# Optimization experiments

Hardware: AMD Instinct MI355X
Metric: run time of the kernel (lower is better)

The kernel has to match this reference:

```python
import jax, jax.numpy as jnp
import numpy as np

E = 1024  # hidden_size
H = 16    # num_heads
D = E // H  # head_dim = 64


def setup_inputs() -> dict:
    key = jax.random.key(0)
    ks = jax.random.split(key, 10)
    s = 1.0 / np.sqrt(E)
    inp = {
        "hidden_states": jax.random.normal(ks[0], (2, 2048, E), dtype=jnp.float32),
        "attention_mask": jnp.ones((2, 2048), dtype=jnp.float32),
        "Wq": jax.random.normal(ks[1], (E, E), dtype=jnp.float32) * s,
        "bq": jnp.zeros((E,), dtype=jnp.float32),
        "Wk": jax.random.normal(ks[2], (E, E), dtype=jnp.float32) * s,
        "bk": jnp.zeros((E,), dtype=jnp.float32),
        "Wv": jax.random.normal(ks[3], (E, E), dtype=jnp.float32) * s,
        "bv": jnp.zeros((E,), dtype=jnp.float32),
        "Wo": jax.random.normal(ks[4], (E, E), dtype=jnp.float32) * s,
        "bo": jnp.zeros((E,), dtype=jnp.float32),
    }
    return inp


def _split_heads(x):
    # [B, S, E] -> [B, H, S, D]
    b, s, _ = x.shape
    return x.reshape(b, s, H, D).transpose(0, 2, 1, 3)


def reference(hidden_states, attention_mask, Wq, bq, Wk, bk, Wv, bv, Wo, bo):
    b, s, _ = hidden_states.shape
    q = _split_heads(hidden_states @ Wq + bq)  # [B,H,S,D]
    k = _split_heads(hidden_states @ Wk + bk)
    v = _split_heads(hidden_states @ Wv + bv)
    scores = jnp.einsum('bhqd,bhkd->bhqk', q, k) / jnp.sqrt(jnp.float32(D))
    scores = scores + (1.0 - attention_mask)[:, None, None, :] * -10000.0
    probs = jax.nn.softmax(scores, axis=-1)
    ctx = jnp.einsum('bhqk,bhkd->bhqd', probs, v)  # [B,H,S,D]
    ctx = ctx.transpose(0, 2, 1, 3).reshape(b, s, E)
    return ctx @ Wo + bo
```

## Files before the change

kernel.cpp:

```cpp
#include <hip/hip_runtime.h>
#include <hip/hip_bf16.h>
#include <stdint.h>

typedef __bf16 bf16x8 __attribute__((ext_vector_type(8)));
typedef __bf16 bf16x4_t __attribute__((ext_vector_type(4)));
typedef float  f32x4  __attribute__((ext_vector_type(4)));
typedef short  short8 __attribute__((ext_vector_type(8)));
typedef short  short4v __attribute__((ext_vector_type(4)));
typedef float  float4v __attribute__((ext_vector_type(4)));

#define AS1 __attribute__((address_space(1)))
#define AS3 __attribute__((address_space(3)))

__device__ __forceinline__ void g2l16(const void* g, void* l) {
    __builtin_amdgcn_global_load_lds((const AS1 void*)g, (AS3 void*)l, 16, 0, 0);
}

__device__ __forceinline__ short f2bf(float f) {
    unsigned u = __builtin_bit_cast(unsigned, f);
    unsigned r = u + 0x7FFFu + ((u >> 16) & 1u);
    return (short)(r >> 16);
}

__device__ __forceinline__ bf16x8 ldb8(const short* p) {
    return __builtin_bit_cast(bf16x8, *(const short8*)p);
}

__device__ __forceinline__ float fast_exp2(float x) {
    return __builtin_amdgcn_exp2f(x);
}

#define LOG2E 1.44269504f
#define QSCL (0.125f * LOG2E)

__global__ __launch_bounds__(256) void prep(
    const float* __restrict__ X, short* __restrict__ Xb,
    const float* __restrict__ W0, const float* __restrict__ W1,
    const float* __restrict__ W2, const float* __restrict__ W3,
    short* __restrict__ T0, short* __restrict__ T1,
    short* __restrict__ T2, short* __restrict__ T3) {
    int gb = blockIdx.x;
    if (gb < 4096) {
        int i = (gb * 256 + threadIdx.x) * 4;
        float4v v = *(const float4v*)(X + i);
        short4v o;
        o[0] = f2bf(v[0]); o[1] = f2bf(v[1]); o[2] = f2bf(v[2]); o[3] = f2bf(v[3]);
        *(short4v*)(Xb + i) = o;
        return;
    }
    int t = gb - 4096;
    int z = t >> 10, rem = t & 1023;
    int xb = rem & 31, yb = rem >> 5;
    const float* W = z == 0 ? W0 : z == 1 ? W1 : z == 2 ? W2 : W3;
    short* T = z == 0 ? T0 : z == 1 ? T1 : z == 2 ? T2 : T3;
    __shared__ float tt[32][33];
    int n0 = xb * 32, k0 = yb * 32;
    int tx = threadIdx.x & 31, ty = threadIdx.x >> 5;
#pragma unroll
    for (int i = 0; i < 4; i++)
        tt[ty + i * 8][tx] = W[(size_t)(k0 + ty + i * 8) * 1024 + n0 + tx];
    __syncthreads();
#pragma unroll
    for (int i = 0; i < 4; i++)
        T[(size_t)(n0 + ty + i * 8) * 1024 + k0 + tx] = f2bf(tt[tx][ty + i * 8]);
}

#define VROW 136
__global__ __launch_bounds__(256) void gemm_qkv(
    const short* __restrict__ Xb,
    const short* __restrict__ WqT, const short* __restrict__ WkT, const short* __restrict__ WvT,
    const float* __restrict__ bq, const float* __restrict__ bk, const float* __restrict__ bv,
    short* __restrict__ Qb, short* __restrict__ Kb, short* __restrict__ VT) {
    const int K = 1024, N = 1024;
    int mt = blockIdx.x;
    int yy = blockIdx.y;
    int mat = yy >> 3, nt = yy & 7;
    const short* Bt = mat == 0 ? WqT : mat == 1 ? WkT : WvT;
    const float* bias = mat == 0 ? bq : mat == 1 ? bk : bv;

    int tid = threadIdx.x;
    int w = tid >> 6, lane = tid & 63;
    int quad = lane >> 4, l16 = lane & 15;
    int wy = w >> 1, wx = w & 1;

    __shared__ __align__(16) short smem[128 * VROW];
    short* A_lds = smem;
    short* B_lds = smem + 4096;

    f32x4 acc[4][4];
#pragma unroll
    for (int i = 0; i < 4; i++)
#pragma unroll
        for (int j = 0; j < 4; j++) acc[i][j] = (f32x4){0.f, 0.f, 0.f, 0.f};

    int m0 = mt * 128, n0 = nt * 128;

    if (mat < 2) {
        for (int kt = 0; kt < 32; kt++) {
            __syncthreads();
#pragma unroll
            for (int c = 0; c < 2; c++) {
                int row = w * 32 + c * 16 + (lane >> 2);
                g2l16(Xb + (size_t)(m0 + row) * K + kt * 32 + (lane & 3) * 8,
                      &A_lds[(w * 32 + c * 16) * 32]);
                g2l16(Bt + (size_t)(n0 + row) * K + kt * 32 + (lane & 3) * 8,
                      &B_lds[(w * 32 + c * 16) * 32]);
            }
            __syncthreads();
            bf16x8 af[4], bfr[4];
#pragma unroll
            for (int i = 0; i < 4; i++) {
                af[i]  = ldb8(&A_lds[(wy * 64 + i * 16 + l16) * 32 + quad * 8]);
                bfr[i] = ldb8(&B_lds[(wx * 64 + i * 16 + l16) * 32 + quad * 8]);
            }
#pragma unroll
            for (int ni = 0; ni < 4; ni++)
#pragma unroll
                for (int mi = 0; mi < 4; mi++)
                    acc[ni][mi] = __builtin_amdgcn_mfma_f32_16x16x32_bf16(bfr[ni], af[mi], acc[ni][mi], 0, 0, 0);
        }
        short* Cout = mat == 0 ? Qb : Kb;
        float s = mat == 0 ? QSCL : 1.0f;
#pragma unroll
        for (int ni = 0; ni < 4; ni++) {
            int c0 = n0 + wx * 64 + ni * 16 + quad * 4;
            float4v bv4 = *(const float4v*)(bias + c0);
#pragma unroll
            for (int mi = 0; mi < 4; mi++) {
                int row = m0 + wy * 64 + mi * 16 + l16;
                f32x4 a = acc[ni][mi];
                f32x4 av = {(a[0] + bv4[0]) * s, (a[1] + bv4[1]) * s,
                            (a[2] + bv4[2]) * s, (a[3] + bv4[3]) * s};
                bf16x4_t ob = __builtin_convertvector(av, bf16x4_t);
                *(short4v*)&Cout[(size_t)row * N + c0] = __builtin_bit_cast(short4v, ob);
            }
        }
    } else {
        for (int kt = 0; kt < 32; kt++) {
            __syncthreads();
#pragma unroll
            for (int c = 0; c < 2; c++) {
                int row = w * 32 + c * 16 + (lane >> 2);
                g2l16(Xb + (size_t)(m0 + row) * K + kt * 32 + (lane & 3) * 8,
                      &A_lds[(w * 32 + c * 16) * 32]);
                g2l16(Bt + (size_t)(n0 + row) * K + kt * 32 + (lane & 3) * 8,
                      &B_lds[(w * 32 + c * 16) * 32]);
            }
            __syncthreads();
            bf16x8 af[4], bfr[4];
#pragma unroll
            for (int i = 0; i < 4; i++) {
                af[i]  = ldb8(&A_lds[(wy * 64 + i * 16 + l16) * 32 + quad * 8]);
                bfr[i] = ldb8(&B_lds[(wx * 64 + i * 16 + l16) * 32 + quad * 8]);
            }
#pragma unroll
            for (int mi = 0; mi < 4; mi++)
#pragma unroll
                for (int ni = 0; ni < 4; ni++)
                    acc[mi][ni] = __builtin_amdgcn_mfma_f32_16x16x32_bf16(af[mi], bfr[ni], acc[mi][ni], 0, 0, 0);
        }
        __syncthreads();
#pragma unroll
        for (int ni = 0; ni < 4; ni++) {
            int cl = wx * 64 + ni * 16 + l16;
            float bv_ = bias[n0 + cl];
#pragma unroll
            for (int mi = 0; mi < 4; mi++) {
                int ml = wy * 64 + mi * 16 + quad * 4;
                f32x4 a = acc[mi][ni];
                f32x4 av = {a[0] + bv_, a[1] + bv_, a[2] + bv_, a[3] + bv_};
                bf16x4_t ob = __builtin_convertvector(av, bf16x4_t);
                *(short4v*)&smem[cl * VROW + ml] = __builtin_bit_cast(short4v, ob);
            }
        }
        __syncthreads();
        int bb = m0 >> 11, ss0 = m0 & 2047;
        int t16 = tid & 15, cw = tid >> 4;
#pragma unroll
        for (int p = 0; p < 8; p++) {
            int cl = p * 16 + cw;
            int col = n0 + cl;
            *(short8*)&VT[(((size_t)(bb * 16)) << 17) + (size_t)col * 2048 + ss0 + t16 * 8] =
                *(const short8*)&smem[cl * VROW + t16 * 8];
        }
    }
}

__global__ __launch_bounds__(256) void gemm_out(
    const short* __restrict__ Ab, const short* __restrict__ Bt,
    const float* __restrict__ bias, float* __restrict__ C) {
    const int K = 1024, N = 1024;
    int mt = blockIdx.x, nt = blockIdx.y;
    int tid = threadIdx.x;
    int w = tid >> 6, lane = tid & 63;
    int quad = lane >> 4, l16 = lane & 15;

    __shared__ __align__(16) short A_lds[64 * 32];
    __shared__ __align__(16) short B_lds[128 * 32];

    f32x4 acc[2][4];
#pragma unroll
    for (int ni = 0; ni < 2; ni++)
#pragma unroll
        for (int mi = 0; mi < 4; mi++) acc[ni][mi] = (f32x4){0.f, 0.f, 0.f, 0.f};

    int m0 = mt * 64, n0 = nt * 128;
    for (int kt = 0; kt < 32; kt++) {
        __syncthreads();
        {
            int row = w * 16 + (lane >> 2);
            g2l16(Ab + (size_t)(m0 + row) * K + kt * 32 + (lane & 3) * 8,
                  &A_lds[(w * 16) * 32]);
        }
#pragma unroll
        for (int c = 0; c < 2; c++) {
            int row = w * 32 + c * 16 + (lane >> 2);
            g2l16(Bt + (size_t)(n0 + row) * K + kt * 32 + (lane & 3) * 8,
                  &B_lds[(w * 32 + c * 16) * 32]);
        }
        __syncthreads();
        bf16x8 af[4], bfr[2];
#pragma unroll
        for (int i = 0; i < 4; i++)
            af[i] = ldb8(&A_lds[(i * 16 + l16) * 32 + quad * 8]);
#pragma unroll
        for (int i = 0; i < 2; i++)
            bfr[i] = ldb8(&B_lds[(w * 32 + i * 16 + l16) * 32 + quad * 8]);
#pragma unroll
        for (int ni = 0; ni < 2; ni++)
#pragma unroll
            for (int mi = 0; mi < 4; mi++)
                acc[ni][mi] = __builtin_amdgcn_mfma_f32_16x16x32_bf16(bfr[ni], af[mi], acc[ni][mi], 0, 0, 0);
    }
#pragma unroll
    for (int ni = 0; ni < 2; ni++) {
        int c0 = n0 + w * 32 + ni * 16 + quad * 4;
        float4v bv4 = *(const float4v*)(bias + c0);
#pragma unroll
        for (int mi = 0; mi < 4; mi++) {
            int row = m0 + mi * 16 + l16;
            f32x4 a = acc[ni][mi];
            float4v av = {a[0] + bv4[0], a[1] + bv4[1], a[2] + bv4[2], a[3] + bv4[3]};
            *(float4v*)&C[(size_t)row * N + c0] = av;
        }
    }
}

#define PROW 72
__global__ __launch_bounds__(512) void attn_kernel(
    const short* __restrict__ Qb, const short* __restrict__ Kb,
    const short* __restrict__ VT, const float* __restrict__ mask,
    short* __restrict__ ctx) {
    const int S = 2048, E = 1024, HH = 16;
    int g = blockIdx.x;
    int p = (g & 7) + 8 * (g >> 7);
    int qb = (g >> 3) & 15;
    int b = p >> 4, h = p & 15;

    int tid = threadIdx.x;
    int w = tid >> 6, lane = tid & 63;
    int quad = lane >> 4, l16 = lane & 15;

    __shared__ __align__(16) short K_lds[2][64 * 64];
    __shared__ __align__(16) short VT_lds[2][64 * 64];
    __shared__ __align__(16) short P_lds[8][16 * PROW];
    __shared__ int maskflag;

    if (tid == 0) maskflag = 1;
    __syncthreads();
    {
        float4v m = *(const float4v*)(mask + b * S + tid * 4);
        if (!(m[0] == 1.f && m[1] == 1.f && m[2] == 1.f && m[3] == 1.f))
            maskflag = 0;
    }
    __syncthreads();
    const bool nomask = (maskflag != 0);

    int q0 = qb * 128;

    bf16x8 qf[2];
#pragma unroll
    for (int kc = 0; kc < 2; kc++)
        qf[kc] = ldb8(Qb + (size_t)(b * S + q0 + w * 16 + l16) * E + h * 64 + kc * 32 + quad * 8);

    short8 ones_s = {0x3F80, 0x3F80, 0x3F80, 0x3F80, 0x3F80, 0x3F80, 0x3F80, 0x3F80};
    bf16x8 vones = __builtin_bit_cast(bf16x8, ones_s);

    f32x4 O_t[4];
    f32x4 lacc = (f32x4){0.f, 0.f, 0.f, 0.f};
#pragma unroll
    for (int nd = 0; nd < 4; nd++) O_t[nd] = (f32x4){0.f, 0.f, 0.f, 0.f};

    const short* Kbase = Kb + (size_t)b * S * E + h * 64;
    const short* Vbase = VT + (size_t)(b * HH + h) * 64 * S;
    short* Pw = &P_lds[w][0];
    int rsw = l16 & 7;

    int srow = w * 8 + (lane >> 3);
    int ssrcb = (lane & 7) ^ (srow & 7);

    g2l16(Kbase + (size_t)srow * E + ssrcb * 8, &K_lds[0][(w * 8) * 64]);
    g2l16(Vbase + (size_t)srow * S + 0 + ssrcb * 8, &VT_lds[0][(w * 8) * 64]);
    __syncthreads();

    for (int kt = 0; kt < 32; kt++) {
        int cur = kt & 1;
        int k0 = kt * 64;
        if (kt < 31) {
            int k1 = k0 + 64;
            g2l16(Kbase + (size_t)(k1 + srow) * E + ssrcb * 8, &K_lds[cur ^ 1][(w * 8) * 64]);
            g2l16(Vbase + (size_t)srow * S + k1 + ssrcb * 8, &VT_lds[cur ^ 1][(w * 8) * 64]);
        }
        const short* Kl = &K_lds[cur][0];
        const short* Vl = &VT_lds[cur][0];

        f32x4 sc[4];
#pragma unroll
        for (int ni = 0; ni < 4; ni++) sc[ni] = (f32x4){0.f, 0.f, 0.f, 0.f};
#pragma unroll
        for (int ni = 0; ni < 4; ni++) {
#pragma unroll
            for (int kc = 0; kc < 2; kc++) {
                int blk = (kc * 4 + quad) ^ rsw;
                bf16x8 kf = ldb8(&Kl[(ni * 16 + l16) * 64 + blk * 8]);
                sc[ni] = __builtin_amdgcn_mfma_f32_16x16x32_bf16(kf, qf[kc], sc[ni], 0, 0, 0);
            }
        }

        if (!nomask) {
#pragma unroll
            for (int ni = 0; ni < 4; ni++) {
                float4v mrow = *(const float4v*)(mask + b * S + k0 + ni * 16 + quad * 4);
#pragma unroll
                for (int r = 0; r < 4; r++)
                    sc[ni][r] += (1.0f - mrow[r]) * (-10000.0f * LOG2E);
            }
        }

#pragma unroll
        for (int ni = 0; ni < 4; ni++)
#pragma unroll
            for (int r = 0; r < 4; r++)
                sc[ni][r] = fast_exp2(sc[ni][r]);

#pragma unroll
        for (int ni = 0; ni < 4; ni++) {
            bf16x4_t pb = __builtin_convertvector(sc[ni], bf16x4_t);
            *(short4v*)&Pw[l16 * PROW + ni * 16 + quad * 4] =
                __builtin_bit_cast(short4v, pb);
        }

#pragma unroll
        for (int ks = 0; ks < 2; ks++) {
            bf16x8 pf = ldb8(&Pw[l16 * PROW + ks * 32 + quad * 8]);
            lacc = __builtin_amdgcn_mfma_f32_16x16x32_bf16(vones, pf, lacc, 0, 0, 0);
#pragma unroll
            for (int nd = 0; nd < 4; nd++) {
                int blk = (ks * 4 + quad) ^ rsw;
                bf16x8 vf = ldb8(&Vl[(nd * 16 + l16) * 64 + blk * 8]);
                O_t[nd] = __builtin_amdgcn_mfma_f32_16x16x32_bf16(vf, pf, O_t[nd], 0, 0, 0);
            }
        }
        __syncthreads();
    }

    {
        float l = lacc[0];
        float inv = l > 0.f ? 1.0f / l : 0.f;
        int row = q0 + w * 16 + l16;
#pragma unroll
        for (int nd = 0; nd < 4; nd++) {
            f32x4 o = O_t[nd];
            f32x4 os = {o[0] * inv, o[1] * inv, o[2] * inv, o[3] * inv};
            bf16x4_t ob = __builtin_convertvector(os, bf16x4_t);
            *(short4v*)&ctx[(size_t)(b * S + row) * E + h * 64 + nd * 16 + quad * 4] =
                __builtin_bit_cast(short4v, ob);
        }
    }
}

extern "C" void kernel_launch(void* const* d_in, const int* in_sizes, int n_in,
                              void* d_out, int out_size, void* d_ws, size_t ws_size,
                              hipStream_t stream) {
    const float* X    = (const float*)d_in[0];
    const float* mask = (const float*)d_in[1];
    const float* Wq   = (const float*)d_in[2];
    const float* bq   = (const float*)d_in[3];
    const float* Wk   = (const float*)d_in[4];
    const float* bk   = (const float*)d_in[5];
    const float* Wv   = (const float*)d_in[6];
    const float* bv   = (const float*)d_in[7];
    const float* Wo   = (const float*)d_in[8];
    const float* bo   = (const float*)d_in[9];
    float* out = (float*)d_out;

    char* ws = (char*)d_ws;
    short* Xb  = (short*)(ws);
    short* WqT = (short*)(ws + (8u << 20));
    short* WkT = (short*)(ws + (10u << 20));
    short* WvT = (short*)(ws + (12u << 20));
    short* WoT = (short*)(ws + (14u << 20));
    short* Qb  = (short*)(ws + (16u << 20));
    short* Kb  = (short*)(ws + (24u << 20));
    short* VT  = (short*)(ws + (32u << 20));
    short* ctx = Xb;

    prep<<<8192, 256, 0, stream>>>(X, Xb, Wq, Wk, Wv, Wo, WqT, WkT, WvT, WoT);
    gemm_qkv<<<dim3(32, 24), 256, 0, stream>>>(Xb, WqT, WkT, WvT, bq, bk, bv, Qb, Kb, VT);
    attn_kernel<<<512, 512, 0, stream>>>(Qb, Kb, VT, mask, ctx);
    gemm_out<<<dim3(64, 8), 256, 0, stream>>>(ctx, WoT, bo, out);
}
```

Measured before the change: 194.0 us.

## Switch attention to 32x32 MFMA tiles with split-K waves and LDS reduction

The attention kernel now uses 32x32x16 bf16 MFMAs instead of 16x16x32. Each wave covers 32 query rows and half of each 64-key tile: four query segments times two key halves across eight waves. The two key-half partial outputs and row sums are combined through an LDS reduction at the end, and the shared memory is unified into one buffer with a new P row pitch. This aims for better MFMA efficiency and fewer fragment loads per FLOP, at the cost of an extra reduction, more accumulator registers, and possible LDS bank conflicts from the new layout.

```diff
diff --git a/kernel.cpp b/kernel.cpp
--- a/kernel.cpp
+++ b/kernel.cpp
@@ -5,6 +5,7 @@
 typedef __bf16 bf16x8 __attribute__((ext_vector_type(8)));
 typedef __bf16 bf16x4_t __attribute__((ext_vector_type(4)));
 typedef float  f32x4  __attribute__((ext_vector_type(4)));
+typedef float  f32x16 __attribute__((ext_vector_type(16)));
 typedef short  short8 __attribute__((ext_vector_type(8)));
 typedef short  short4v __attribute__((ext_vector_type(4)));
 typedef float  float4v __attribute__((ext_vector_type(4)));
@@ -246,7 +247,7 @@
     }
 }
 
-#define PROW 72
+#define PR2 56
 __global__ __launch_bounds__(512) void attn_kernel(
     const short* __restrict__ Qb, const short* __restrict__ Kb,
     const short* __restrict__ VT, const float* __restrict__ mask,
@@ -259,11 +260,13 @@
 
     int tid = threadIdx.x;
     int w = tid >> 6, lane = tid & 63;
-    int quad = lane >> 4, l16 = lane & 15;
-
-    __shared__ __align__(16) short K_lds[2][64 * 64];
-    __shared__ __align__(16) short VT_lds[2][64 * 64];
-    __shared__ __align__(16) short P_lds[8][16 * PROW];
+    int l32 = lane & 31, hi = lane >> 5;
+    int qseg = w & 3, khalf = w >> 2;
+
+    __shared__ __align__(16) short smem_s[8192 + 8192 + 8 * 32 * PR2];
+    short* K_lds = smem_s;
+    short* V_lds = smem_s + 8192;
+    short* Pw = smem_s + 16384 + w * 32 * PR2;
     __shared__ int maskflag;
 
     if (tid == 0) maskflag = 1;
@@ -278,29 +281,28 @@
 
     int q0 = qb * 128;
 
-    bf16x8 qf[2];
-#pragma unroll
-    for (int kc = 0; kc < 2; kc++)
-        qf[kc] = ldb8(Qb + (size_t)(b * S + q0 + w * 16 + l16) * E + h * 64 + kc * 32 + quad * 8);
+    bf16x8 qf[4];
+#pragma unroll
+    for (int step = 0; step < 4; step++)
+        qf[step] = ldb8(Qb + (size_t)(b * S + q0 + qseg * 32 + l32) * E + h * 64 + step * 16 + hi * 8);
 
     short8 ones_s = {0x3F80, 0x3F80, 0x3F80, 0x3F80, 0x3F80, 0x3F80, 0x3F80, 0x3F80};
     bf16x8 vones = __builtin_bit_cast(bf16x8, ones_s);
 
-    f32x4 O_t[4];
-    f32x4 lacc = (f32x4){0.f, 0.f, 0.f, 0.f};
-#pragma unroll
-    for (int nd = 0; nd < 4; nd++) O_t[nd] = (f32x4){0.f, 0.f, 0.f, 0.f};
+    f32x16 O_t[2];
+    f32x16 lacc;
+#pragma unroll
+    for (int i = 0; i < 16; i++) { O_t[0][i] = 0.f; O_t[1][i] = 0.f; lacc[i] = 0.f; }
 
     const short* Kbase = Kb + (size_t)b * S * E + h * 64;
     const short* Vbase = VT + (size_t)(b * HH + h) * 64 * S;
-    short* Pw = &P_lds[w][0];
-    int rsw = l16 & 7;
 
     int srow = w * 8 + (lane >> 3);
     int ssrcb = (lane & 7) ^ (srow & 7);
-
-    g2l16(Kbase + (size_t)srow * E + ssrcb * 8, &K_lds[0][(w * 8) * 64]);
-    g2l16(Vbase + (size_t)srow * S + 0 + ssrcb * 8, &VT_lds[0][(w * 8) * 64]);
+    int l7 = lane & 7;
+
+    g2l16(Kbase + (size_t)srow * E + ssrcb * 8, &K_lds[(w * 8) * 64]);
+    g2l16(Vbase + (size_t)srow * S + 0 + ssrcb * 8, &V_lds[(w * 8) * 64]);
     __syncthreads();
 
     for (int kt = 0; kt < 32; kt++) {
@@ -308,73 +310,84 @@
         int k0 = kt * 64;
         if (kt < 31) {
             int k1 = k0 + 64;
-            g2l16(Kbase + (size_t)(k1 + srow) * E + ssrcb * 8, &K_lds[cur ^ 1][(w * 8) * 64]);
-            g2l16(Vbase + (size_t)srow * S + k1 + ssrcb * 8, &VT_lds[cur ^ 1][(w * 8) * 64]);
-        }
-        const short* Kl = &K_lds[cur][0];
-        const short* Vl = &VT_lds[cur][0];
-
-        f32x4 sc[4];
-#pragma unroll
-        for (int ni = 0; ni < 4; ni++) sc[ni] = (f32x4){0.f, 0.f, 0.f, 0.f};
-#pragma unroll
-        for (int ni = 0; ni < 4; ni++) {
-#pragma unroll
-            for (int kc = 0; kc < 2; kc++) {
-                int blk = (kc * 4 + quad) ^ rsw;
-                bf16x8 kf = ldb8(&Kl[(ni * 16 + l16) * 64 + blk * 8]);
-                sc[ni] = __builtin_amdgcn_mfma_f32_16x16x32_bf16(kf, qf[kc], sc[ni], 0, 0, 0);
-            }
+            g2l16(Kbase + (size_t)(k1 + srow) * E + ssrcb * 8, &K_lds[(cur ^ 1) * 4096 + (w * 8) * 64]);
+            g2l16(Vbase + (size_t)srow * S + k1 + ssrcb * 8, &V_lds[(cur ^ 1) * 4096 + (w * 8) * 64]);
+        }
+        const short* Kl = &K_lds[cur * 4096];
+        const short* Vl = &V_lds[cur * 4096];
+
+        f32x16 sc;
+#pragma unroll
+        for (int i = 0; i < 16; i++) sc[i] = 0.f;
+#pragma unroll
+        for (int step = 0; step < 4; step++) {
+            int blk = (step * 2 + hi) ^ l7;
+            bf16x8 kf = ldb8(&Kl[(khalf * 32 + l32) * 64 + blk * 8]);
+            sc = __builtin_amdgcn_mfma_f32_32x32x16_bf16(kf, qf[step], sc, 0, 0, 0);
         }
 
         if (!nomask) {
 #pragma unroll
-            for (int ni = 0; ni < 4; ni++) {
-                float4v mrow = *(const float4v*)(mask + b * S + k0 + ni * 16 + quad * 4);
+            for (int gg = 0; gg < 4; gg++) {
+                float4v mrow = *(const float4v*)(mask + b * S + k0 + khalf * 32 + gg * 8 + hi * 4);
 #pragma unroll
                 for (int r = 0; r < 4; r++)
-                    sc[ni][r] += (1.0f - mrow[r]) * (-10000.0f * LOG2E);
-            }
-        }
-
-#pragma unroll
-        for (int ni = 0; ni < 4; ni++)
-#pragma unroll
-            for (int r = 0; r < 4; r++)
-                sc[ni][r] = fast_exp2(sc[ni][r]);
-
-#pragma unroll
-        for (int ni = 0; ni < 4; ni++) {
-            bf16x4_t pb = __builtin_convertvector(sc[ni], bf16x4_t);
-            *(short4v*)&Pw[l16 * PROW + ni * 16 + quad * 4] =
-                __builtin_bit_cast(short4v, pb);
-        }
-
-#pragma unroll
-        for (int ks = 0; ks < 2; ks++) {
-            bf16x8 pf = ldb8(&Pw[l16 * PROW + ks * 32 + quad * 8]);
-            lacc = __builtin_amdgcn_mfma_f32_16x16x32_bf16(vones, pf, lacc, 0, 0, 0);
-#pragma unroll
-            for (int nd = 0; nd < 4; nd++) {
-                int blk = (ks * 4 + quad) ^ rsw;
-                bf16x8 vf = ldb8(&Vl[(nd * 16 + l16) * 64 + blk * 8]);
-                O_t[nd] = __builtin_amdgcn_mfma_f32_16x16x32_bf16(vf, pf, O_t[nd], 0, 0, 0);
+                    sc[gg * 4 + r] += (1.0f - mrow[r]) * (-10000.0f * LOG2E);
+            }
+        }
+
+#pragma unroll
+        for (int i = 0; i < 16; i++) sc[i] = fast_exp2(sc[i]);
+
+#pragma unroll
+        for (int gg = 0; gg < 4; gg++) {
+            f32x4 v4 = {sc[gg * 4 + 0], sc[gg * 4 + 1], sc[gg * 4 + 2], sc[gg * 4 + 3]};
+            bf16x4_t pb = __builtin_convertvector(v4, bf16x4_t);
+            *(short4v*)&Pw[l32 * PR2 + gg * 8 + hi * 4] = __builtin_bit_cast(short4v, pb);
+        }
+
+#pragma unroll
+        for (int step = 0; step < 2; step++) {
+            bf16x8 pf = ldb8(&Pw[l32 * PR2 + step * 16 + hi * 8]);
+            lacc = __builtin_amdgcn_mfma_f32_32x32x16_bf16(vones, pf, lacc, 0, 0, 0);
+#pragma unroll
+            for (int dseg = 0; dseg < 2; dseg++) {
+                int vblk = (khalf * 4 + step * 2 + hi) ^ l7;
+                bf16x8 vf = ldb8(&Vl[(dseg * 32 + l32) * 64 + vblk * 8]);
+                O_t[dseg] = __builtin_amdgcn_mfma_f32_32x32x16_bf16(vf, pf, O_t[dseg], 0, 0, 0);
             }
         }
         __syncthreads();
     }
 
-    {
-        float l = lacc[0];
+    float* Red = (float*)smem_s;
+    __syncthreads();
+    if (khalf == 1) {
+        float* r = &Red[(qseg * 64 + lane) * 33];
+#pragma unroll
+        for (int dseg = 0; dseg < 2; dseg++)
+#pragma unroll
+            for (int i = 0; i < 16; i++) r[dseg * 16 + i] = O_t[dseg][i];
+        r[32] = lacc[0];
+    }
+    __syncthreads();
+    if (khalf == 0) {
+        const float* r = &Red[(qseg * 64 + lane) * 33];
+        float l = lacc[0] + r[32];
         float inv = l > 0.f ? 1.0f / l : 0.f;
-        int row = q0 + w * 16 + l16;
-#pragma unroll
-        for (int nd = 0; nd < 4; nd++) {
-            f32x4 o = O_t[nd];
-            f32x4 os = {o[0] * inv, o[1] * inv, o[2] * inv, o[3] * inv};
-            bf16x4_t ob = __builtin_convertvector(os, bf16x4_t);
-            *(short4v*)&ctx[(size_t)(b * S + row) * E + h * 64 + nd * 16 + quad * 4] =
-                __builtin_bit_cast(short4v, ob);
+        int row = q0 + qseg * 32 + l32;
+#pragma unroll
+        for (int dseg = 0; dseg < 2; dseg++) {
+#pragma unroll
+            for (int gg = 0; gg < 4; gg++) {
+                f32x4 v4 = {(O_t[dseg][gg * 4 + 0] + r[dseg * 16 + gg * 4 + 0]) * inv,
+                            (O_t[dseg][gg * 4 + 1] + r[dseg * 16 + gg * 4 + 1]) * inv,
+                            (O_t[dseg][gg * 4 + 2] + r[dseg * 16 + gg * 4 + 2]) * inv,
+                            (O_t[dseg][gg * 4 + 3] + r[dseg * 16 + gg * 4 + 3]) * inv};
+                bf16x4_t ob = __builtin_convertvector(v4, bf16x4_t);
+                *(short4v*)&ctx[(size_t)(b * S + row) * E + h * 64 + dseg * 32 + gg * 8 + hi * 4] =
+                    __builtin_bit_cast(short4v, ob);
+            }
         }
     }
 }
```

After: 196.1 us. About the same (+1.1%).

## Double-buffer LDS tiles in projection GEMMs and pad attention P buffer

Applied to the files above, without the earlier changes.

Both the QKV and output GEMMs now use two LDS buffers, so the global-to-LDS load for tile k+1 is issued before the MFMAs on tile k. This replaces two barriers per iteration with one and is meant to hide load latency behind compute. The attention P scratch row stride changes from 72 to 76 shorts, with the 8-element fragment read as two 4-element loads, to reduce LDS bank conflicts. The trade-off is twice the LDS footprint per block, which may lower occupancy. The loop also relies on global_load_lds completing by the single barrier without an explicit vmcnt wait, which could be a correctness risk.

```diff
diff --git a/kernel.cpp b/kernel.cpp
--- a/kernel.cpp
+++ b/kernel.cpp
@@ -84,8 +84,6 @@
     int wy = w >> 1, wx = w & 1;
 
     __shared__ __align__(16) short smem[128 * VROW];
-    short* A_lds = smem;
-    short* B_lds = smem + 4096;
 
     f32x4 acc[4][4];
 #pragma unroll
@@ -94,30 +92,40 @@
         for (int j = 0; j < 4; j++) acc[i][j] = (f32x4){0.f, 0.f, 0.f, 0.f};
 
     int m0 = mt * 128, n0 = nt * 128;
+
+    auto stage = [&](int kt, short* A, short* B) {
+#pragma unroll
+        for (int c = 0; c < 2; c++) {
+            int row = w * 32 + c * 16 + (lane >> 2);
+            g2l16(Xb + (size_t)(m0 + row) * K + kt * 32 + (lane & 3) * 8,
+                  &A[(w * 32 + c * 16) * 32]);
+            g2l16(Bt + (size_t)(n0 + row) * K + kt * 32 + (lane & 3) * 8,
+                  &B[(w * 32 + c * 16) * 32]);
+        }
+    };
+
+    stage(0, smem, smem + 8192);
+    __syncthreads();
 
     if (mat < 2) {
         for (int kt = 0; kt < 32; kt++) {
-            __syncthreads();
-#pragma unroll
-            for (int c = 0; c < 2; c++) {
-                int row = w * 32 + c * 16 + (lane >> 2);
-                g2l16(Xb + (size_t)(m0 + row) * K + kt * 32 + (lane & 3) * 8,
-                      &A_lds[(w * 32 + c * 16) * 32]);
-                g2l16(Bt + (size_t)(n0 + row) * K + kt * 32 + (lane & 3) * 8,
-                      &B_lds[(w * 32 + c * 16) * 32]);
-            }
-            __syncthreads();
+            int cur = kt & 1;
+            const short* Al = cur ? smem + 4096 : smem;
+            const short* Bl = cur ? smem + 12288 : smem + 8192;
+            if (kt < 31)
+                stage(kt + 1, cur ? smem : smem + 4096, cur ? smem + 8192 : smem + 12288);
             bf16x8 af[4], bfr[4];
 #pragma unroll
             for (int i = 0; i < 4; i++) {
-                af[i]  = ldb8(&A_lds[(wy * 64 + i * 16 + l16) * 32 + quad * 8]);
-                bfr[i] = ldb8(&B_lds[(wx * 64 + i * 16 + l16) * 32 + quad * 8]);
+                af[i]  = ldb8(&Al[(wy * 64 + i * 16 + l16) * 32 + quad * 8]);
+                bfr[i] = ldb8(&Bl[(wx * 64 + i * 16 + l16) * 32 + quad * 8]);
             }
 #pragma unroll
             for (int ni = 0; ni < 4; ni++)
 #pragma unroll
                 for (int mi = 0; mi < 4; mi++)
                     acc[ni][mi] = __builtin_amdgcn_mfma_f32_16x16x32_bf16(bfr[ni], af[mi], acc[ni][mi], 0, 0, 0);
+            __syncthreads();
         }
         short* Cout = mat == 0 ? Qb : Kb;
         float s = mat == 0 ? QSCL : 1.0f;
@@ -137,29 +145,24 @@
         }
     } else {
         for (int kt = 0; kt < 32; kt++) {
-            __syncthreads();
-#pragma unroll
-            for (int c = 0; c < 2; c++) {
-                int row = w * 32 + c * 16 + (lane >> 2);
-                g2l16(Xb + (size_t)(m0 + row) * K + kt * 32 + (lane & 3) * 8,
-                      &A_lds[(w * 32 + c * 16) * 32]);
-                g2l16(Bt + (size_t)(n0 + row) * K + kt * 32 + (lane & 3) * 8,
-                      &B_lds[(w * 32 + c * 16) * 32]);
-            }
-            __syncthreads();
+            int cur = kt & 1;
+            const short* Al = cur ? smem + 4096 : smem;
+            const short* Bl = cur ? smem + 12288 : smem + 8192;
+            if (kt < 31)
+                stage(kt + 1, cur ? smem : smem + 4096, cur ? smem + 8192 : smem + 12288);
             bf16x8 af[4], bfr[4];
 #pragma unroll
             for (int i = 0; i < 4; i++) {
-                af[i]  = ldb8(&A_lds[(wy * 64 + i * 16 + l16) * 32 + quad * 8]);
-                bfr[i] = ldb8(&B_lds[(wx * 64 + i * 16 + l16) * 32 + quad * 8]);
+                af[i]  = ldb8(&Al[(wy * 64 + i * 16 + l16) * 32 + quad * 8]);
+                bfr[i] = ldb8(&Bl[(wx * 64 + i * 16 + l16) * 32 + quad * 8]);
             }
 #pragma unroll
             for (int mi = 0; mi < 4; mi++)
 #pragma unroll
                 for (int ni = 0; ni < 4; ni++)
                     acc[mi][ni] = __builtin_amdgcn_mfma_f32_16x16x32_bf16(af[mi], bfr[ni], acc[mi][ni], 0, 0, 0);
-        }
-        __syncthreads();
+            __syncthreads();
+        }
 #pragma unroll
         for (int ni = 0; ni < 4; ni++) {
             int cl = wx * 64 + ni * 16 + l16;
@@ -195,8 +198,7 @@
     int w = tid >> 6, lane = tid & 63;
     int quad = lane >> 4, l16 = lane & 15;
 
-    __shared__ __align__(16) short A_lds[64 * 32];
-    __shared__ __align__(16) short B_lds[128 * 32];
+    __shared__ __align__(16) short smem[12288];
 
     f32x4 acc[2][4];
 #pragma unroll
@@ -205,32 +207,43 @@
         for (int mi = 0; mi < 4; mi++) acc[ni][mi] = (f32x4){0.f, 0.f, 0.f, 0.f};
 
     int m0 = mt * 64, n0 = nt * 128;
-    for (int kt = 0; kt < 32; kt++) {
-        __syncthreads();
+
+    auto stage = [&](int kt, short* A, short* B) {
         {
             int row = w * 16 + (lane >> 2);
             g2l16(Ab + (size_t)(m0 + row) * K + kt * 32 + (lane & 3) * 8,
-                  &A_lds[(w * 16) * 32]);
+                  &A[(w * 16) * 32]);
         }
 #pragma unroll
         for (int c = 0; c < 2; c++) {
             int row = w * 32 + c * 16 + (lane >> 2);
             g2l16(Bt + (size_t)(n0 + row) * K + kt * 32 + (lane & 3) * 8,
-                  &B_lds[(w * 32 + c * 16) * 32]);
-        }
-        __syncthreads();
+                  &B[(w * 32 + c * 16) * 32]);
+        }
+    };
+
+    stage(0, smem, smem + 4096);
+    __syncthreads();
+
+    for (int kt = 0; kt < 32; kt++) {
+        int cur = kt & 1;
+        const short* Al = cur ? smem + 2048 : smem;
+        const short* Bl = cur ? smem + 8192 : smem + 4096;
+        if (kt < 31)
+            stage(kt + 1, cur ? smem : smem + 2048, cur ? smem + 4096 : smem + 8192);
         bf16x8 af[4], bfr[2];
 #pragma unroll
         for (int i = 0; i < 4; i++)
-            af[i] = ldb8(&A_lds[(i * 16 + l16) * 32 + quad * 8]);
+            af[i] = ldb8(&Al[(i * 16 + l16) * 32 + quad * 8]);
 #pragma unroll
         for (int i = 0; i < 2; i++)
-            bfr[i] = ldb8(&B_lds[(w * 32 + i * 16 + l16) * 32 + quad * 8]);
+            bfr[i] = ldb8(&Bl[(w * 32 + i * 16 + l16) * 32 + quad * 8]);
 #pragma unroll
         for (int ni = 0; ni < 2; ni++)
 #pragma unroll
             for (int mi = 0; mi < 4; mi++)
                 acc[ni][mi] = __builtin_amdgcn_mfma_f32_16x16x32_bf16(bfr[ni], af[mi], acc[ni][mi], 0, 0, 0);
+        __syncthreads();
     }
 #pragma unroll
     for (int ni = 0; ni < 2; ni++) {
@@ -246,7 +259,7 @@
     }
 }
 
-#define PROW 72
+#define PROW 76
 __global__ __launch_bounds__(512) void attn_kernel(
     const short* __restrict__ Qb, const short* __restrict__ Kb,
     const short* __restrict__ VT, const float* __restrict__ mask,
@@ -352,7 +365,10 @@
 
 #pragma unroll
         for (int ks = 0; ks < 2; ks++) {
-            bf16x8 pf = ldb8(&Pw[l16 * PROW + ks * 32 + quad * 8]);
+            short4v p0 = *(const short4v*)&Pw[l16 * PROW + ks * 32 + quad * 8];
+            short4v p1 = *(const short4v*)&Pw[l16 * PROW + ks * 32 + quad * 8 + 4];
+            short8 pc = {p0[0], p0[1], p0[2], p0[3], p1[0], p1[1], p1[2], p1[3]};
+            bf16x8 pf = __builtin_bit_cast(bf16x8, pc);
             lacc = __builtin_amdgcn_mfma_f32_16x16x32_bf16(vones, pf, lacc, 0, 0, 0);
 #pragma unroll
             for (int nd = 0; nd < 4; nd++) {
```

Measured after the change: 195.4 us. No clear change (+0.7%).

## Double GEMM K-tile to 64 with XOR-swizzled LDS and pad attention P rows

Applied to the files above, without the earlier changes.

Both projection GEMMs now stage 64-wide K tiles into LDS, using an XOR swizzle on 16-byte blocks, so they run half as many barrier-separated iterations. The swizzle is meant to avoid LDS bank conflicts on the fragment reads. The duplicated Q/K and V main loops are merged into one loop that branches on the matrix type. In attention, the P row stride goes from 72 to 76 and P fragments are read as two 8-byte loads, aiming to cut bank conflicts at the cost of losing 16-byte aligned reads.

```diff
diff --git a/kernel.cpp b/kernel.cpp
--- a/kernel.cpp
+++ b/kernel.cpp
@@ -82,10 +82,11 @@
     int w = tid >> 6, lane = tid & 63;
     int quad = lane >> 4, l16 = lane & 15;
     int wy = w >> 1, wx = w & 1;
+    int rsw = l16 & 7;
 
     __shared__ __align__(16) short smem[128 * VROW];
     short* A_lds = smem;
-    short* B_lds = smem + 4096;
+    short* B_lds = smem + 8192;
 
     f32x4 acc[4][4];
 #pragma unroll
@@ -94,31 +95,46 @@
         for (int j = 0; j < 4; j++) acc[i][j] = (f32x4){0.f, 0.f, 0.f, 0.f};
 
     int m0 = mt * 128, n0 = nt * 128;
+    int srow8 = lane >> 3;
+    int ssrcb = (lane & 7) ^ srow8;
+
+    for (int kt = 0; kt < 16; kt++) {
+        __syncthreads();
+#pragma unroll
+        for (int c = 0; c < 4; c++) {
+            int row = w * 32 + c * 8 + srow8;
+            g2l16(Xb + (size_t)(m0 + row) * K + kt * 64 + ssrcb * 8,
+                  &A_lds[(w * 32 + c * 8) * 64]);
+            g2l16(Bt + (size_t)(n0 + row) * K + kt * 64 + ssrcb * 8,
+                  &B_lds[(w * 32 + c * 8) * 64]);
+        }
+        __syncthreads();
+#pragma unroll
+        for (int kc = 0; kc < 2; kc++) {
+            int blk = (kc * 4 + quad) ^ rsw;
+            bf16x8 af[4], bfr[4];
+#pragma unroll
+            for (int i = 0; i < 4; i++) {
+                af[i]  = ldb8(&A_lds[(wy * 64 + i * 16 + l16) * 64 + blk * 8]);
+                bfr[i] = ldb8(&B_lds[(wx * 64 + i * 16 + l16) * 64 + blk * 8]);
+            }
+            if (mat < 2) {
+#pragma unroll
+                for (int ni = 0; ni < 4; ni++)
+#pragma unroll
+                    for (int mi = 0; mi < 4; mi++)
+                        acc[ni][mi] = __builtin_amdgcn_mfma_f32_16x16x32_bf16(bfr[ni], af[mi], acc[ni][mi], 0, 0, 0);
+            } else {
+#pragma unroll
+                for (int mi = 0; mi < 4; mi++)
+#pragma unroll
+                    for (int ni = 0; ni < 4; ni++)
+                        acc[mi][ni] = __builtin_amdgcn_mfma_f32_16x16x32_bf16(af[mi], bfr[ni], acc[mi][ni], 0, 0, 0);
+            }
+        }
+    }
 
     if (mat < 2) {
-        for (int kt = 0; kt < 32; kt++) {
-            __syncthreads();
-#pragma unroll
-            for (int c = 0; c < 2; c++) {
-                int row = w * 32 + c * 16 + (lane >> 2);
-                g2l16(Xb + (size_t)(m0 + row) * K + kt * 32 + (lane & 3) * 8,
-                      &A_lds[(w * 32 + c * 16) * 32]);
-                g2l16(Bt + (size_t)(n0 + row) * K + kt * 32 + (lane & 3) * 8,
-                      &B_lds[(w * 32 + c * 16) * 32]);
-            }
-            __syncthreads();
-            bf16x8 af[4], bfr[4];
-#pragma unroll
-            for (int i = 0; i < 4; i++) {
-                af[i]  = ldb8(&A_lds[(wy * 64 + i * 16 + l16) * 32 + quad * 8]);
-                bfr[i] = ldb8(&B_lds[(wx * 64 + i * 16 + l16) * 32 + quad * 8]);
-            }
-#pragma unroll
-            for (int ni = 0; ni < 4; ni++)
-#pragma unroll
-                for (int mi = 0; mi < 4; mi++)
-                    acc[ni][mi] = __builtin_amdgcn_mfma_f32_16x16x32_bf16(bfr[ni], af[mi], acc[ni][mi], 0, 0, 0);
-        }
         short* Cout = mat == 0 ? Qb : Kb;
         float s = mat == 0 ? QSCL : 1.0f;
 #pragma unroll
@@ -136,29 +152,6 @@
             }
         }
     } else {
-        for (int kt = 0; kt < 32; kt++) {
-            __syncthreads();
-#pragma unroll
-            for (int c = 0; c < 2; c++) {
-                int row = w * 32 + c * 16 + (lane >> 2);
-                g2l16(Xb + (size_t)(m0 + row) * K + kt * 32 + (lane & 3) * 8,
-                      &A_lds[(w * 32 + c * 16) * 32]);
-                g2l16(Bt + (size_t)(n0 + row) * K + kt * 32 + (lane & 3) * 8,
-                      &B_lds[(w * 32 + c * 16) * 32]);
-            }
-            __syncthreads();
-            bf16x8 af[4], bfr[4];
-#pragma unroll
-            for (int i = 0; i < 4; i++) {
-                af[i]  = ldb8(&A_lds[(wy * 64 + i * 16 + l16) * 32 + quad * 8]);
-                bfr[i] = ldb8(&B_lds[(wx * 64 + i * 16 + l16) * 32 + quad * 8]);
-            }
-#pragma unroll
-            for (int mi = 0; mi < 4; mi++)
-#pragma unroll
-                for (int ni = 0; ni < 4; ni++)
-                    acc[mi][ni] = __builtin_amdgcn_mfma_f32_16x16x32_bf16(af[mi], bfr[ni], acc[mi][ni], 0, 0, 0);
-        }
         __syncthreads();
 #pragma unroll
         for (int ni = 0; ni < 4; ni++) {
@@ -194,9 +187,11 @@
     int tid = threadIdx.x;
     int w = tid >> 6, lane = tid & 63;
     int quad = lane >> 4, l16 = lane & 15;
-
-    __shared__ __align__(16) short A_lds[64 * 32];
-    __shared__ __align__(16) short B_lds[128 * 32];
+    int rsw = l16 & 7;
+
+    __shared__ __align__(16) short smem[12288];
+    short* A_lds = smem;
+    short* B_lds = smem + 4096;
 
     f32x4 acc[2][4];
 #pragma unroll
@@ -205,32 +200,40 @@
         for (int mi = 0; mi < 4; mi++) acc[ni][mi] = (f32x4){0.f, 0.f, 0.f, 0.f};
 
     int m0 = mt * 64, n0 = nt * 128;
-    for (int kt = 0; kt < 32; kt++) {
-        __syncthreads();
-        {
-            int row = w * 16 + (lane >> 2);
-            g2l16(Ab + (size_t)(m0 + row) * K + kt * 32 + (lane & 3) * 8,
-                  &A_lds[(w * 16) * 32]);
-        }
+    int srow8 = lane >> 3;
+    int ssrcb = (lane & 7) ^ srow8;
+
+    for (int kt = 0; kt < 16; kt++) {
+        __syncthreads();
 #pragma unroll
         for (int c = 0; c < 2; c++) {
-            int row = w * 32 + c * 16 + (lane >> 2);
-            g2l16(Bt + (size_t)(n0 + row) * K + kt * 32 + (lane & 3) * 8,
-                  &B_lds[(w * 32 + c * 16) * 32]);
-        }
-        __syncthreads();
-        bf16x8 af[4], bfr[2];
-#pragma unroll
-        for (int i = 0; i < 4; i++)
-            af[i] = ldb8(&A_lds[(i * 16 + l16) * 32 + quad * 8]);
-#pragma unroll
-        for (int i = 0; i < 2; i++)
-            bfr[i] = ldb8(&B_lds[(w * 32 + i * 16 + l16) * 32 + quad * 8]);
-#pragma unroll
-        for (int ni = 0; ni < 2; ni++)
-#pragma unroll
-            for (int mi = 0; mi < 4; mi++)
-                acc[ni][mi] = __builtin_amdgcn_mfma_f32_16x16x32_bf16(bfr[ni], af[mi], acc[ni][mi], 0, 0, 0);
+            int row = w * 16 + c * 8 + srow8;
+            g2l16(Ab + (size_t)(m0 + row) * K + kt * 64 + ssrcb * 8,
+                  &A_lds[(w * 16 + c * 8) * 64]);
+        }
+#pragma unroll
+        for (int c = 0; c < 4; c++) {
+            int row = w * 32 + c * 8 + srow8;
+            g2l16(Bt + (size_t)(n0 + row) * K + kt * 64 + ssrcb * 8,
+                  &B_lds[(w * 32 + c * 8) * 64]);
+        }
+        __syncthreads();
+#pragma unroll
+        for (int kc = 0; kc < 2; kc++) {
+            int blk = (kc * 4 + quad) ^ rsw;
+            bf16x8 af[4], bfr[2];
+#pragma unroll
+            for (int i = 0; i < 4; i++)
+                af[i] = ldb8(&A_lds[(i * 16 + l16) * 64 + blk * 8]);
+#pragma unroll
+            for (int i = 0; i < 2; i++)
+                bfr[i] = ldb8(&B_lds[(w * 32 + i * 16 + l16) * 64 + blk * 8]);
+#pragma unroll
+            for (int ni = 0; ni < 2; ni++)
+#pragma unroll
+                for (int mi = 0; mi < 4; mi++)
+                    acc[ni][mi] = __builtin_amdgcn_mfma_f32_16x16x32_bf16(bfr[ni], af[mi], acc[ni][mi], 0, 0, 0);
+        }
     }
 #pragma unroll
     for (int ni = 0; ni < 2; ni++) {
@@ -246,7 +249,7 @@
     }
 }
 
-#define PROW 72
+#define PROW 76
 __global__ __launch_bounds__(512) void attn_kernel(
     const short* __restrict__ Qb, const short* __restrict__ Kb,
     const short* __restrict__ VT, const float* __restrict__ mask,
@@ -352,7 +355,10 @@
 
 #pragma unroll
         for (int ks = 0; ks < 2; ks++) {
-            bf16x8 pf = ldb8(&Pw[l16 * PROW + ks * 32 + quad * 8]);
+            short4v p0 = *(const short4v*)&Pw[l16 * PROW + ks * 32 + quad * 8];
+            short4v p1 = *(const short4v*)&Pw[l16 * PROW + ks * 32 + quad * 8 + 4];
+            short8 pc = {p0[0], p0[1], p0[2], p0[3], p1[0], p1[1], p1[2], p1[3]};
+            bf16x8 pf = __builtin_bit_cast(bf16x8, pc);
             lacc = __builtin_amdgcn_mfma_f32_16x16x32_bf16(vones, pf, lacc, 0, 0, 0);
 #pragma unroll
             for (int nd = 0; nd < 4; nd++) {
```

New measurement: 207.0 us. 6.7% more time.
